# Kernel tuning notes

Measured on AMD Instinct MI355X. Metric: run time of the kernel, lower is better.

Reference implementation:

```python
import jax, jax.numpy as jnp
import numpy as np

B, NX, NY, E, H, L = 4, 1024, 1024, 512, 8, 4
DH = E // H
FF = 4 * E
SCALE = DH ** (-0.5)
EPS = 1e-5


def _ln(x, g, b):
    mu = jnp.mean(x, axis=-1, keepdims=True)
    var = jnp.mean((x - mu) ** 2, axis=-1, keepdims=True)
    return (x - mu) * jax.lax.rsqrt(var + EPS) * g + b


def setup_inputs() -> dict:
    key = jax.random.key(0)
    ks = jax.random.split(key, 16)
    s = 0.02
    inp = {
        'x': jax.random.normal(ks[0], (B, NX, E), jnp.float32),
        'y': jax.random.normal(ks[1], (B, NY, E), jnp.float32),
        'x_mask': jax.random.randint(ks[2], (B, NX), 0, 2, jnp.int32),
        'y_mask': jax.random.randint(ks[3], (B, NY), 0, 2, jnp.int32),
        # stacked per-layer params (L leading dim)
        'Wq': jax.random.normal(ks[4], (L, E, E), jnp.float32) * s,
        'bq': jnp.zeros((L, E), jnp.float32),
        'Wk': jax.random.normal(ks[5], (L, E, E), jnp.float32) * s,
        'bk': jnp.zeros((L, E), jnp.float32),
        'Wv': jax.random.normal(ks[6], (L, E, E), jnp.float32) * s,
        'bv': jnp.zeros((L, E), jnp.float32),
        'Wo': jax.random.normal(ks[7], (L, E, E), jnp.float32) * s,
        'bo': jnp.zeros((L, E), jnp.float32),
        'g1': jnp.ones((L, E), jnp.float32),
        'be1': jnp.zeros((L, E), jnp.float32),
        'g2': jnp.ones((L, E), jnp.float32),
        'be2': jnp.zeros((L, E), jnp.float32),
        'W1': jax.random.normal(ks[8], (L, E, FF), jnp.float32) * s,
        'bf1': jnp.zeros((L, FF), jnp.float32),
        'W2': jax.random.normal(ks[9], (L, FF, E), jnp.float32) * s,
        'bf2': jnp.zeros((L, E), jnp.float32),
    }
    return inp


def _forward(x, y, mask4, Wq, bq, Wk, bk, Wv, bv, Wo, bo, g1, be1, g2, be2, W1, bf1, W2, bf2):
    # mask4: (B,1,NX,NY) int, 0 = masked
    attn_prev = None
    out = x
    for l in range(L):
        q = x @ Wq[l] + bq[l]              # (B,NX,E)
        k = y @ Wk[l] + bk[l]
        v = y @ Wv[l] + bv[l]
        # faithful non-standard head split: plain reshape, no transpose
        q = q.reshape(B, H, NX, DH)
        k = k.reshape(B, H, NY, DH)
        v = v.reshape(B, H, NY, DH)
        scores = jnp.einsum('bhnd,bhmd->bhnm', q, k) * SCALE
        scores = jnp.where(mask4 == 0, jnp.float32(-1e9), scores)
        a = jax.nn.softmax(scores, axis=-1)
        if attn_prev is not None:
            a = a + attn_prev  # residual attention
        attn_prev = a
        o = jnp.einsum('bhnm,bhmd->bhnd', a, v)
        o = jnp.transpose(o, (0, 2, 1, 3)).reshape(B, NX, E)
        o = o @ Wo[l] + bo[l]
        h = _ln(x + o, g1[l], be1[l])
        ff = jax.nn.gelu(h @ W1[l] + bf1[l], approximate=False) @ W2[l] + bf2[l]
        out = _ln(h + ff, g2[l], be2[l])
        # NOTE: faithful to source, x and y are NOT updated between layers;
        # only the attention residual chains. Final output is last layer's out.
    return out


def reference(x, y, x_mask, y_mask, Wq, bq, Wk, bk, Wv, bv, Wo, bo, g1, be1, g2, be2, W1, bf1, W2, bf2):
    mask4 = (x_mask[:, :, None].astype(jnp.float32) @ y_mask[:, None, :].astype(jnp.float32)).astype(jnp.int32)[:, None]
    return _forward(x, y, mask4, Wq, bq, Wk, bk, Wv, bv, Wo, bo, g1, be1, g2, be2, W1, bf1, W2, bf2)
```

## Files before the change

kernel.cpp:

```cpp
#include <hip/hip_runtime.h>
#include <cstdint>

using u16    = unsigned short;
using u32    = unsigned int;
using bf16x8 = __attribute__((ext_vector_type(8))) __bf16;
using f32x4  = __attribute__((ext_vector_type(4))) float;

__device__ __forceinline__ u16 f2bf(float f) {
    u32 u = __builtin_bit_cast(u32, f);
    u += 0x7FFFu + ((u >> 16) & 1u);
    return (u16)(u >> 16);
}
__device__ __forceinline__ float bf2f(u16 u) {
    return __builtin_bit_cast(float, (u32)u << 16);
}
__device__ __forceinline__ u32 pk_bf16(float a, float b) {
    u32 r;
    asm("v_cvt_pk_bf16_f32 %0, %1, %2" : "=v"(r) : "v"(a), "v"(b));
    return r;
}
__device__ __forceinline__ float hw_exp2(float x) {
    float r;
    asm("v_exp_f32 %0, %1" : "=v"(r) : "v"(x));
    return r;
}
__device__ __forceinline__ void load_lds16(const u16* g, u16* l) {
    __builtin_amdgcn_global_load_lds((const __attribute__((address_space(1))) void*)g,
                                     (__attribute__((address_space(3))) void*)l, 16, 0, 0);
}

__global__ __launch_bounds__(256) void cvt2_kernel(const float* __restrict__ a,
                                                   const float* __restrict__ b,
                                                   u16* __restrict__ oa,
                                                   u16* __restrict__ ob)
{
    const int bid = blockIdx.x;
    const float* in = bid < 2048 ? a : b;
    u16* out = bid < 2048 ? oa : ob;
    int i = ((bid & 2047) * 256 + threadIdx.x) * 4;
    float4 v = *(const float4*)(in + i);
    uint2 o;
    o.x = (u32)f2bf(v.x) | ((u32)f2bf(v.y) << 16);
    o.y = (u32)f2bf(v.z) | ((u32)f2bf(v.w) << 16);
    *(uint2*)(out + i) = o;
}

__global__ __launch_bounds__(256) void wtrans_kernel(const float* __restrict__ Wq,
                                                     const float* __restrict__ Wk,
                                                     const float* __restrict__ Wv,
                                                     const float* __restrict__ Wo,
                                                     const float* __restrict__ W1,
                                                     const float* __restrict__ W2,
                                                     u16* __restrict__ wt)
{
    const int gid = blockIdx.x;
    const float* src; u16* dst; int K = 512, N = 512; int n0, k0;
    if (gid < 2560) {
        int z = gid >> 8, tid = gid & 255;
        switch (z) {
            case 0: case 1: case 2: case 3:
                src = Wq + (size_t)z * 262144;        dst = wt + (size_t)z * 262144;            break;
            case 4: case 5: case 6: case 7:
                src = Wk + (size_t)(z - 4) * 262144;  dst = wt + 1048576 + (size_t)(z - 4) * 262144; break;
            case 8: src = Wv + 3 * 262144;  dst = wt + 2097152; break;
            default: src = Wo + 3 * 262144; dst = wt + 2359296; break;
        }
        n0 = (tid & 15) * 32; k0 = (tid >> 4) * 32;
    } else if (gid < 3584) {
        int tid = gid - 2560;
        src = W1 + 3 * 1048576; dst = wt + 2621440; K = 512; N = 2048;
        n0 = (tid & 63) * 32; k0 = (tid >> 6) * 32;
    } else {
        int tid = gid - 3584;
        src = W2 + 3 * 1048576; dst = wt + 3670016; K = 2048; N = 512;
        n0 = (tid & 15) * 32; k0 = (tid >> 4) * 32;
    }
    __shared__ float tile[32][33];
    int tx = threadIdx.x, ty = threadIdx.y;
    #pragma unroll
    for (int i = 0; i < 4; i++) {
        int r = ty + i * 8;
        tile[r][tx] = src[(size_t)(k0 + r) * N + n0 + tx];
    }
    __syncthreads();
    #pragma unroll
    for (int i = 0; i < 4; i++) {
        int rn = ty + i * 8;
        dst[(size_t)(n0 + rn) * K + k0 + tx] = f2bf(tile[tx][rn]);
    }
}

template<int BNF>
__device__ __forceinline__ void gemm_core32(const u16* __restrict__ A,
                                            const u16* __restrict__ BT,
                                            int K, int m0, int n0,
                                            u16 (*As)[32], u16 (*Bs)[32],
                                            f32x4 acc[4][BNF])
{
    const int t    = threadIdx.x;
    const int lane = t & 63, wid = t >> 6;
    const int wm = wid >> 1, wn = wid & 1;
    const int lrow = lane & 15, kg = lane >> 4;
    const int sr = lane >> 2;
    const int sg = ((lane & 3) ^ ((lane >> 3) & 3)) * 8;

    auto stage = [&](int buf, int ks) {
        #pragma unroll
        for (int i = 0; i < 2; i++) {
            int row = wid * 32 + i * 16;
            load_lds16(&A[(size_t)(m0 + row + sr) * K + ks + sg], &As[buf * 128 + row][0]);
        }
        if constexpr (BNF == 4) {
            #pragma unroll
            for (int i = 0; i < 2; i++) {
                int row = wid * 32 + i * 16;
                load_lds16(&BT[(size_t)(n0 + row + sr) * K + ks + sg], &Bs[buf * 128 + row][0]);
            }
        } else {
            int row = wid * 16;
            load_lds16(&BT[(size_t)(n0 + row + sr) * K + ks + sg], &Bs[buf * 64 + row][0]);
        }
    };

    stage(0, 0);
    __syncthreads();
    int buf = 0;
    for (int ks = 0; ks < K; ks += 32) {
        if (ks + 32 < K) stage(buf ^ 1, ks + 32);
        const int rg = (kg ^ ((lrow >> 1) & 3)) * 8;
        bf16x8 af[4], bfv[BNF];
        #pragma unroll
        for (int i = 0; i < 4; i++)
            af[i] = *(const bf16x8*)&As[buf * 128 + wm * 64 + i * 16 + lrow][rg];
        #pragma unroll
        for (int j = 0; j < BNF; j++)
            bfv[j] = *(const bf16x8*)&Bs[buf * (BNF * 32) + wn * (BNF * 16) + j * 16 + lrow][rg];
        #pragma unroll
        for (int i = 0; i < 4; i++)
            #pragma unroll
            for (int j = 0; j < BNF; j++)
                acc[i][j] = __builtin_amdgcn_mfma_f32_16x16x32_bf16(af[i], bfv[j], acc[i][j], 0, 0, 0);
        __syncthreads();
        buf ^= 1;
    }
}

__global__ __launch_bounds__(256) void qkv_gemm_kernel(const u16* __restrict__ x16,
                                                       const u16* __restrict__ y16,
                                                       const u16* __restrict__ wt,
                                                       u16* __restrict__ qkv,
                                                       const float* __restrict__ bq,
                                                       const float* __restrict__ bk,
                                                       const float* __restrict__ bv,
                                                       const int* __restrict__ x_mask)
{
    __shared__ u16 As[256][32];
    __shared__ u16 Bs[256][32];
    const int z = blockIdx.z;
    const u16* A; const u16* BT; const float* bias;
    if (z < 4)      { A = x16; BT = wt + (size_t)z * 262144;                 bias = bq + z * 512; }
    else if (z < 8) { A = y16; BT = wt + 1048576 + (size_t)(z - 4) * 262144; bias = bk + (z - 4) * 512; }
    else            { A = y16; BT = wt + 2097152;                            bias = bv + 3 * 512; }
    u16* out = qkv + (size_t)z * 2097152;

    const int m0 = blockIdx.y * 128, n0 = blockIdx.x * 128;
    f32x4 acc[4][4];
    #pragma unroll
    for (int i = 0; i < 4; i++)
        #pragma unroll
        for (int j = 0; j < 4; j++) acc[i][j] = f32x4{0.f, 0.f, 0.f, 0.f};
    gemm_core32<4>(A, BT, 512, m0, n0, As, Bs, acc);

    const int lane = threadIdx.x & 63, wid = threadIdx.x >> 6;
    const int wm = wid >> 1, wn = wid & 1;
    const int lrow = lane & 15, kg = lane >> 4;
    #pragma unroll
    for (int i = 0; i < 4; i++)
        #pragma unroll
        for (int j = 0; j < 4; j++)
            #pragma unroll
            for (int r = 0; r < 4; r++) {
                int row = m0 + wm * 64 + i * 16 + kg * 4 + r;
                int col = n0 + wn * 64 + j * 16 + lrow;
                float v = acc[i][j][r] + bias[col];
                if (z < 4) v *= 0.180336880f * (x_mask[row] ? 1.f : 0.f);
                out[(size_t)row * 512 + col] = f2bf(v);
            }
}

template<int BNF, int EPI>
__global__ __launch_bounds__(256) void gemm_bt_kernel(const u16* __restrict__ A,
                                                      const u16* __restrict__ BT,
                                                      const float* __restrict__ bias,
                                                      void* __restrict__ outp,
                                                      const float* __restrict__ res,
                                                      int N, int K)
{
    __shared__ u16 As[256][32];
    __shared__ u16 Bs[BNF * 64][32];
    const int m0 = blockIdx.y * 128, n0 = blockIdx.x * (BNF * 32);
    f32x4 acc[4][BNF];
    #pragma unroll
    for (int i = 0; i < 4; i++)
        #pragma unroll
        for (int j = 0; j < BNF; j++) acc[i][j] = f32x4{0.f, 0.f, 0.f, 0.f};
    gemm_core32<BNF>(A, BT, K, m0, n0, As, Bs, acc);

    const int lane = threadIdx.x & 63, wid = threadIdx.x >> 6;
    const int wm = wid >> 1, wn = wid & 1;
    const int lrow = lane & 15, kg = lane >> 4;
    #pragma unroll
    for (int i = 0; i < 4; i++)
        #pragma unroll
        for (int j = 0; j < BNF; j++)
            #pragma unroll
            for (int r = 0; r < 4; r++) {
                int row = m0 + wm * 64 + i * 16 + kg * 4 + r;
                int col = n0 + wn * (BNF * 16) + j * 16 + lrow;
                float v = acc[i][j][r] + bias[col];
                if constexpr (EPI == 1) {
                    ((float*)outp)[(size_t)row * N + col] = v + res[(size_t)row * N + col];
                } else {
                    v = 0.5f * v * (1.f + erff(v * 0.70710678118654752f));
                    ((u16*)outp)[(size_t)row * N + col] = f2bf(v);
                }
            }
}

__global__ __launch_bounds__(256) void vtrans_kernel(const u16* __restrict__ v, u16* __restrict__ vt)
{
    const int bh = blockIdx.y, m0 = blockIdx.x * 64;
    const int b = bh >> 3, h = bh & 7;
    const u16* src = v + (size_t)b * 524288 + (size_t)h * 65536;
    u16* dst = vt + (size_t)bh * 65536;
    __shared__ u16 tile[64][72];
    const int t = threadIdx.x;
    #pragma unroll
    for (int i = 0; i < 2; i++) {
        int idx = t + i * 256, r = idx >> 3, q = idx & 7;
        *(uint4*)&tile[r][q * 8] = *(const uint4*)&src[(size_t)(m0 + r) * 64 + q * 8];
    }
    __syncthreads();
    #pragma unroll
    for (int i = 0; i < 2; i++) {
        int idx = t + i * 256, d = idx >> 3, q = idx & 7;
        alignas(16) u16 tmp[8];
        #pragma unroll
        for (int j = 0; j < 8; j++) tmp[j] = tile[q * 8 + j][d];
        *(uint4*)&dst[(size_t)d * 1024 + m0 + q * 8] = *(uint4*)tmp;
    }
}

__global__ __launch_bounds__(256, 2) void attn_kernel(const u16* __restrict__ qkv,
                                                      const int* __restrict__ x_mask,
                                                      const int* __restrict__ y_mask,
                                                      const u16* __restrict__ vt,
                                                      u16* __restrict__ obuf)
{
    __shared__ __align__(16) char smem[45056];
    u16 (*Kb)[4][32][64] = reinterpret_cast<u16(*)[4][32][64]>(smem);
    u16 (*Vb)[64][32]    = reinterpret_cast<u16(*)[64][32]>(smem + 32768);
    float* ymb           = reinterpret_cast<float*>(smem + 40960);
    u16 (*Osh)[64][72]   = reinterpret_cast<u16(*)[64][72]>(smem);

    const int t = threadIdx.x;
    const int wid = t >> 6, lane = t & 63;
    const int lrow = lane & 15, kg = lane >> 4;

    const int gid  = blockIdx.x;
    const int orig = (gid & 7) * 64 + (gid >> 3);
    const int bh = orig >> 4, qt = orig & 15;
    const int b = bh >> 3, h = bh & 7;
    const int q0 = qt * 64;

    const size_t headoff = (size_t)b * 524288 + (size_t)h * 65536;
    const u16* Q  = qkv + (size_t)wid * 2097152 + headoff;
    const u16* VT = vt + (size_t)bh * 65536;

    for (int i = t; i < 1024; i += 256)
        ymb[i] = y_mask[b * 1024 + i] ? 0.f : -1e9f;

    const int ksrow = wid * 8 + (lane >> 3);
    const int kscol = ((lane & 7) ^ (lane >> 3)) * 8;
    const int vsrow = wid * 16 + (lane >> 2);
    const int vscol = (((lane & 3) ^ ((vsrow & 3) ^ ((vsrow >> 2) & 3))) * 8);
    const int fswz  = (lrow & 3) ^ ((lrow >> 2) & 3);

    auto stage = [&](int buf, int mt) {
        const int m0 = mt * 32;
        #pragma unroll
        for (int it = 0; it < 4; it++) {
            const u16* src = qkv + (size_t)(4 + it) * 2097152 + headoff
                           + (size_t)(m0 + ksrow) * 64 + kscol;
            load_lds16(src, &Kb[buf][it][wid * 8][0]);
        }
        load_lds16(&VT[(size_t)vsrow * 1024 + m0 + vscol], &Vb[buf][wid * 16][0]);
    };

    bf16x8 aq[4][2];
    #pragma unroll
    for (int i = 0; i < 4; i++) {
        aq[i][0] = *(const bf16x8*)&Q[(size_t)(q0 + i * 16 + lrow) * 64 + kg * 8];
        aq[i][1] = *(const bf16x8*)&Q[(size_t)(q0 + i * 16 + lrow) * 64 + 32 + kg * 8];
    }
    float xmf[4];
    #pragma unroll
    for (int i = 0; i < 4; i++) xmf[i] = x_mask[b * 1024 + q0 + i * 16 + lrow] ? 1.f : 0.f;

    const int srcA = (((2 * kg) & 3) << 4) | lrow;
    const int srcB = (((2 * kg + 1) & 3) << 4) | lrow;

    f32x4 oacc[4][4];
    float psum[4] = {0.f, 0.f, 0.f, 0.f};
    #pragma unroll
    for (int i = 0; i < 4; i++)
        #pragma unroll
        for (int d = 0; d < 4; d++) oacc[i][d] = f32x4{0.f, 0.f, 0.f, 0.f};

    stage(0, 0);
    __syncthreads();

    for (int mt = 0; mt < 32; mt++) {
        const int buf = mt & 1;
        const int m0 = mt * 32;
        if (mt < 31) stage(buf ^ 1, mt + 1);

        bf16x8 kb[2][2];
        #pragma unroll
        for (int nf = 0; nf < 2; nf++)
            #pragma unroll
            for (int kk = 0; kk < 2; kk++)
                kb[nf][kk] = *(const bf16x8*)&Kb[buf][wid][nf * 16 + lrow][((kk * 4 + kg) ^ (lrow & 7)) * 8];

        float yb[2][4];
        #pragma unroll
        for (int nf = 0; nf < 2; nf++)
            #pragma unroll
            for (int r = 0; r < 4; r++) yb[nf][r] = ymb[m0 + nf * 16 + kg * 4 + r];

        bf16x8 pa[4];
        #pragma unroll
        for (int i = 0; i < 4; i++) {
            f32x4 s0 = f32x4{0.f, 0.f, 0.f, 0.f}, s1 = f32x4{0.f, 0.f, 0.f, 0.f};
            s0 = __builtin_amdgcn_mfma_f32_16x16x32_bf16(kb[0][0], aq[i][0], s0, 0, 0, 0);
            s0 = __builtin_amdgcn_mfma_f32_16x16x32_bf16(kb[0][1], aq[i][1], s0, 0, 0, 0);
            s1 = __builtin_amdgcn_mfma_f32_16x16x32_bf16(kb[1][0], aq[i][0], s1, 0, 0, 0);
            s1 = __builtin_amdgcn_mfma_f32_16x16x32_bf16(kb[1][1], aq[i][1], s1, 0, 0, 0);
            float p0 = hw_exp2(fmaf(xmf[i], yb[0][0], s0[0]));
            float p1 = hw_exp2(fmaf(xmf[i], yb[0][1], s0[1]));
            float p2 = hw_exp2(fmaf(xmf[i], yb[0][2], s0[2]));
            float p3 = hw_exp2(fmaf(xmf[i], yb[0][3], s0[3]));
            float p4 = hw_exp2(fmaf(xmf[i], yb[1][0], s1[0]));
            float p5 = hw_exp2(fmaf(xmf[i], yb[1][1], s1[1]));
            float p6 = hw_exp2(fmaf(xmf[i], yb[1][2], s1[2]));
            float p7 = hw_exp2(fmaf(xmf[i], yb[1][3], s1[3]));
            psum[i] += ((p0 + p1) + (p2 + p3)) + ((p4 + p5) + (p6 + p7));
            u32 w0 = pk_bf16(p0, p1), w1 = pk_bf16(p2, p3);
            u32 w2 = pk_bf16(p4, p5), w3 = pk_bf16(p6, p7);
            u32 a0 = __shfl(w0, srcA), a1 = __shfl(w1, srcA);
            u32 a2 = __shfl(w0, srcB), a3 = __shfl(w1, srcB);
            u32 b0 = __shfl(w2, srcA), b1 = __shfl(w3, srcA);
            u32 b2 = __shfl(w2, srcB), b3 = __shfl(w3, srcB);
            const bool hi = (kg & 2) != 0;
            uint4 pw;
            pw.x = hi ? b0 : a0;
            pw.y = hi ? b1 : a1;
            pw.z = hi ? b2 : a2;
            pw.w = hi ? b3 : a3;
            pa[i] = __builtin_bit_cast(bf16x8, pw);
        }

        bf16x8 vbf[4];
        #pragma unroll
        for (int d = 0; d < 4; d++)
            vbf[d] = *(const bf16x8*)&Vb[buf][d * 16 + lrow][(kg ^ fswz) * 8];
        #pragma unroll
        for (int i = 0; i < 4; i++)
            #pragma unroll
            for (int d = 0; d < 4; d++)
                oacc[i][d] = __builtin_amdgcn_mfma_f32_16x16x32_bf16(pa[i], vbf[d], oacc[i][d], 0, 0, 0);

        __syncthreads();
    }

    #pragma unroll
    for (int i = 0; i < 4; i++) {
        psum[i] += __shfl_xor(psum[i], 16);
        psum[i] += __shfl_xor(psum[i], 32);
    }
    float invr[4][4];
    #pragma unroll
    for (int i = 0; i < 4; i++) {
        float inv = 1.f / psum[i];
        #pragma unroll
        for (int r = 0; r < 4; r++) invr[i][r] = __shfl(inv, kg * 4 + r, 16);
    }

    #pragma unroll
    for (int i = 0; i < 4; i++)
        #pragma unroll
        for (int d = 0; d < 4; d++)
            #pragma unroll
            for (int r = 0; r < 4; r++)
                Osh[wid][i * 16 + kg * 4 + r][d * 16 + lrow] = f2bf(oacc[i][d][r] * invr[i][r]);
    __syncthreads();

    {
        const int row = t >> 2, cbase = (t & 3) * 16;
        #pragma unroll
        for (int half = 0; half < 2; half++) {
            const int c0 = cbase + half * 8;
            float a8[8] = {0, 0, 0, 0, 0, 0, 0, 0};
            #pragma unroll
            for (int l = 0; l < 4; l++) {
                uint4 v = *(const uint4*)&Osh[l][row][c0];
                const u16* pv = (const u16*)&v;
                #pragma unroll
                for (int j = 0; j < 8; j++) a8[j] += bf2f(pv[j]);
            }
            alignas(16) u16 tmp[8];
            #pragma unroll
            for (int j = 0; j < 8; j++) tmp[j] = f2bf(a8[j]);
            *(uint4*)&obuf[(size_t)(b * 1024 + q0 + row) * 512 + h * 64 + c0] = *(uint4*)tmp;
        }
    }
}

template<int MODE>
__global__ __launch_bounds__(256) void ln_kernel(const float* __restrict__ in,
                                                 const float* __restrict__ g,
                                                 const float* __restrict__ be,
                                                 float* __restrict__ out32,
                                                 u16* __restrict__ out16)
{
    const int wid = threadIdx.x >> 6, lane = threadIdx.x & 63;
    const int row = blockIdx.x * 4 + wid;
    const float* x = in + (size_t)row * 512;
    float4 v1 = *(const float4*)&x[lane * 8];
    float4 v2 = *(const float4*)&x[lane * 8 + 4];
    float xv[8] = { v1.x, v1.y, v1.z, v1.w, v2.x, v2.y, v2.z, v2.w };
    float s = 0.f, s2 = 0.f;
    #pragma unroll
    for (int j = 0; j < 8; j++) { s += xv[j]; s2 += xv[j] * xv[j]; }
    #pragma unroll
    for (int off = 32; off > 0; off >>= 1) {
        s  += __shfl_xor(s, off, 64);
        s2 += __shfl_xor(s2, off, 64);
    }
    const float mean = s * (1.f / 512.f);
    const float var  = s2 * (1.f / 512.f) - mean * mean;
    const float rstd = rsqrtf(var + 1e-5f);
    float ov[8];
    #pragma unroll
    for (int j = 0; j < 8; j++) {
        int col = lane * 8 + j;
        ov[j] = (xv[j] - mean) * rstd * g[col] + be[col];
    }
    *(float4*)&out32[(size_t)row * 512 + lane * 8]     = float4{ ov[0], ov[1], ov[2], ov[3] };
    *(float4*)&out32[(size_t)row * 512 + lane * 8 + 4] = float4{ ov[4], ov[5], ov[6], ov[7] };
    if constexpr (MODE == 0) {
        alignas(16) u16 tmp[8];
        #pragma unroll
        for (int j = 0; j < 8; j++) tmp[j] = f2bf(ov[j]);
        *(uint4*)&out16[(size_t)row * 512 + lane * 8] = *(uint4*)tmp;
    }
}

extern "C" void kernel_launch(void* const* d_in, const int* in_sizes, int n_in,
                              void* d_out, int out_size, void* d_ws, size_t ws_size,
                              hipStream_t stream) {
    const float* x      = (const float*)d_in[0];
    const float* y      = (const float*)d_in[1];
    const int*   x_mask = (const int*)d_in[2];
    const int*   y_mask = (const int*)d_in[3];
    const float* Wq  = (const float*)d_in[4];
    const float* bq  = (const float*)d_in[5];
    const float* Wk  = (const float*)d_in[6];
    const float* bk  = (const float*)d_in[7];
    const float* Wv  = (const float*)d_in[8];
    const float* bv  = (const float*)d_in[9];
    const float* Wo  = (const float*)d_in[10];
    const float* bo  = (const float*)d_in[11];
    const float* g1  = (const float*)d_in[12];
    const float* be1 = (const float*)d_in[13];
    const float* g2  = (const float*)d_in[14];
    const float* be2 = (const float*)d_in[15];
    const float* W1  = (const float*)d_in[16];
    const float* bf1 = (const float*)d_in[17];
    const float* W2  = (const float*)d_in[18];
    const float* bf2 = (const float*)d_in[19];

    char* p = (char*)d_ws;
    auto alloc = [&](size_t bytes) { char* r = p; p += (bytes + 255) & ~(size_t)255; return r; };
    u16*   x16   = (u16*)alloc(2097152ULL * 2);
    u16*   y16   = (u16*)alloc(2097152ULL * 2);
    u16*   wt    = (u16*)alloc(4718592ULL * 2);
    u16*   qkv   = (u16*)alloc(9ULL * 2097152 * 2);
    u16*   vt    = (u16*)alloc(2097152ULL * 2);
    u16*   obuf  = (u16*)alloc(2097152ULL * 2);
    float* xo    = (float*)alloc(2097152ULL * 4);
    float* h32   = (float*)alloc(2097152ULL * 4);
    u16*   h16   = (u16*)alloc(2097152ULL * 2);
    u16*   ffmid = (u16*)alloc(8388608ULL * 2);
    float* ffout = (float*)alloc(2097152ULL * 4);
    if ((size_t)(p - (char*)d_ws) > ws_size) return;

    cvt2_kernel<<<4096, 256, 0, stream>>>(x, y, x16, y16);
    wtrans_kernel<<<4608, dim3(32, 8), 0, stream>>>(Wq, Wk, Wv, Wo, W1, W2, wt);
    qkv_gemm_kernel<<<dim3(4, 32, 9), 256, 0, stream>>>(x16, y16, wt, qkv, bq, bk, bv, x_mask);
    vtrans_kernel<<<dim3(16, 32), 256, 0, stream>>>(qkv + 8ULL * 2097152, vt);
    attn_kernel<<<512, 256, 0, stream>>>(qkv, x_mask, y_mask, vt, obuf);
    gemm_bt_kernel<2, 1><<<dim3(8, 32), 256, 0, stream>>>(obuf, wt + 2359296, bo + 3 * 512, xo, x, 512, 512);
    ln_kernel<0><<<1024, 256, 0, stream>>>(xo, g1 + 3 * 512, be1 + 3 * 512, h32, h16);
    gemm_bt_kernel<4, 2><<<dim3(16, 32), 256, 0, stream>>>(h16, wt + 2621440, bf1 + 3 * 2048, ffmid, nullptr, 2048, 512);
    gemm_bt_kernel<2, 1><<<dim3(8, 32), 256, 0, stream>>>(ffmid, wt + 3670016, bf2 + 3 * 512, ffout, h32, 512, 2048);
    ln_kernel<1><<<1024, 256, 0, stream>>>(ffout, g2 + 3 * 512, be2 + 3 * 512, (float*)d_out, nullptr);
}
```

Before: 185.8 us.

## Split attention block into 8 waves covering two query halves

The attention kernel now launches 512 threads per block: each of four layer-waves is duplicated across two 32-row query halves, so each wave holds half the Q fragments and accumulators. K staging is spread over all 8 waves, and V staging uses only the first four. The final cross-layer sum is re-indexed so each thread reduces one 8-wide slice. This is meant to raise wave-level parallelism and cut per-wave register pressure. In exchange, K/V LDS reads are duplicated across the two query halves and the block barriers cover more waves.

```diff
diff --git a/kernel.cpp b/kernel.cpp
--- a/kernel.cpp
+++ b/kernel.cpp
@@ -251,21 +251,23 @@
     }
 }
 
-__global__ __launch_bounds__(256, 2) void attn_kernel(const u16* __restrict__ qkv,
-                                                      const int* __restrict__ x_mask,
-                                                      const int* __restrict__ y_mask,
-                                                      const u16* __restrict__ vt,
-                                                      u16* __restrict__ obuf)
+__global__ __launch_bounds__(512) void attn_kernel(const u16* __restrict__ qkv,
+                                                   const int* __restrict__ x_mask,
+                                                   const int* __restrict__ y_mask,
+                                                   const u16* __restrict__ vt,
+                                                   u16* __restrict__ obuf)
 {
     __shared__ __align__(16) char smem[45056];
     u16 (*Kb)[4][32][64] = reinterpret_cast<u16(*)[4][32][64]>(smem);
     u16 (*Vb)[64][32]    = reinterpret_cast<u16(*)[64][32]>(smem + 32768);
     float* ymb           = reinterpret_cast<float*>(smem + 40960);
-    u16 (*Osh)[64][72]   = reinterpret_cast<u16(*)[64][72]>(smem);
+    u16 (*Osh)[32][72]   = reinterpret_cast<u16(*)[32][72]>(smem);
 
     const int t = threadIdx.x;
     const int wid = t >> 6, lane = t & 63;
     const int lrow = lane & 15, kg = lane >> 4;
+    const int L  = wid & 3;
+    const int qh = wid >> 2;
 
     const int gid  = blockIdx.x;
     const int orig = (gid & 7) * 64 + (gid >> 3);
@@ -274,13 +276,12 @@
     const int q0 = qt * 64;
 
     const size_t headoff = (size_t)b * 524288 + (size_t)h * 65536;
-    const u16* Q  = qkv + (size_t)wid * 2097152 + headoff;
+    const u16* Q  = qkv + (size_t)L * 2097152 + headoff;
     const u16* VT = vt + (size_t)bh * 65536;
 
-    for (int i = t; i < 1024; i += 256)
+    for (int i = t; i < 1024; i += 512)
         ymb[i] = y_mask[b * 1024 + i] ? 0.f : -1e9f;
 
-    const int ksrow = wid * 8 + (lane >> 3);
     const int kscol = ((lane & 7) ^ (lane >> 3)) * 8;
     const int vsrow = wid * 16 + (lane >> 2);
     const int vscol = (((lane & 3) ^ ((vsrow & 3) ^ ((vsrow >> 2) & 3))) * 8);
@@ -288,32 +289,38 @@
 
     auto stage = [&](int buf, int mt) {
         const int m0 = mt * 32;
-        #pragma unroll
-        for (int it = 0; it < 4; it++) {
+        u16* kbase = &Kb[buf][0][0][0];
+        #pragma unroll
+        for (int i = 0; i < 2; i++) {
+            const int fr = i * 64 + wid * 8 + (lane >> 3);
+            const int it = fr >> 5, r = fr & 31;
             const u16* src = qkv + (size_t)(4 + it) * 2097152 + headoff
-                           + (size_t)(m0 + ksrow) * 64 + kscol;
-            load_lds16(src, &Kb[buf][it][wid * 8][0]);
+                           + (size_t)(m0 + r) * 64 + kscol;
+            load_lds16(src, kbase + (i * 512 + wid * 64) * 8);
         }
-        load_lds16(&VT[(size_t)vsrow * 1024 + m0 + vscol], &Vb[buf][wid * 16][0]);
+        if (wid < 4)
+            load_lds16(&VT[(size_t)vsrow * 1024 + m0 + vscol], &Vb[buf][wid * 16][0]);
     };
 
-    bf16x8 aq[4][2];
-    #pragma unroll
-    for (int i = 0; i < 4; i++) {
-        aq[i][0] = *(const bf16x8*)&Q[(size_t)(q0 + i * 16 + lrow) * 64 + kg * 8];
-        aq[i][1] = *(const bf16x8*)&Q[(size_t)(q0 + i * 16 + lrow) * 64 + 32 + kg * 8];
-    }
-    float xmf[4];
-    #pragma unroll
-    for (int i = 0; i < 4; i++) xmf[i] = x_mask[b * 1024 + q0 + i * 16 + lrow] ? 1.f : 0.f;
+    bf16x8 aq[2][2];
+    #pragma unroll
+    for (int i = 0; i < 2; i++) {
+        const int qr = q0 + qh * 32 + i * 16 + lrow;
+        aq[i][0] = *(const bf16x8*)&Q[(size_t)qr * 64 + kg * 8];
+        aq[i][1] = *(const bf16x8*)&Q[(size_t)qr * 64 + 32 + kg * 8];
+    }
+    float xmf[2];
+    #pragma unroll
+    for (int i = 0; i < 2; i++)
+        xmf[i] = x_mask[b * 1024 + q0 + qh * 32 + i * 16 + lrow] ? 1.f : 0.f;
 
     const int srcA = (((2 * kg) & 3) << 4) | lrow;
     const int srcB = (((2 * kg + 1) & 3) << 4) | lrow;
 
-    f32x4 oacc[4][4];
-    float psum[4] = {0.f, 0.f, 0.f, 0.f};
-    #pragma unroll
-    for (int i = 0; i < 4; i++)
+    f32x4 oacc[2][4];
+    float psum[2] = {0.f, 0.f};
+    #pragma unroll
+    for (int i = 0; i < 2; i++)
         #pragma unroll
         for (int d = 0; d < 4; d++) oacc[i][d] = f32x4{0.f, 0.f, 0.f, 0.f};
 
@@ -330,7 +337,7 @@
         for (int nf = 0; nf < 2; nf++)
             #pragma unroll
             for (int kk = 0; kk < 2; kk++)
-                kb[nf][kk] = *(const bf16x8*)&Kb[buf][wid][nf * 16 + lrow][((kk * 4 + kg) ^ (lrow & 7)) * 8];
+                kb[nf][kk] = *(const bf16x8*)&Kb[buf][L][nf * 16 + lrow][((kk * 4 + kg) ^ (lrow & 7)) * 8];
 
         float yb[2][4];
         #pragma unroll
@@ -338,9 +345,9 @@
             #pragma unroll
             for (int r = 0; r < 4; r++) yb[nf][r] = ymb[m0 + nf * 16 + kg * 4 + r];
 
-        bf16x8 pa[4];
-        #pragma unroll
-        for (int i = 0; i < 4; i++) {
+        bf16x8 pa[2];
+        #pragma unroll
+        for (int i = 0; i < 2; i++) {
             f32x4 s0 = f32x4{0.f, 0.f, 0.f, 0.f}, s1 = f32x4{0.f, 0.f, 0.f, 0.f};
             s0 = __builtin_amdgcn_mfma_f32_16x16x32_bf16(kb[0][0], aq[i][0], s0, 0, 0, 0);
             s0 = __builtin_amdgcn_mfma_f32_16x16x32_bf16(kb[0][1], aq[i][1], s0, 0, 0, 0);
@@ -375,7 +382,7 @@
         for (int d = 0; d < 4; d++)
             vbf[d] = *(const bf16x8*)&Vb[buf][d * 16 + lrow][(kg ^ fswz) * 8];
         #pragma unroll
-        for (int i = 0; i < 4; i++)
+        for (int i = 0; i < 2; i++)
             #pragma unroll
             for (int d = 0; d < 4; d++)
                 oacc[i][d] = __builtin_amdgcn_mfma_f32_16x16x32_bf16(pa[i], vbf[d], oacc[i][d], 0, 0, 0);
@@ -384,20 +391,20 @@
     }
 
     #pragma unroll
-    for (int i = 0; i < 4; i++) {
+    for (int i = 0; i < 2; i++) {
         psum[i] += __shfl_xor(psum[i], 16);
         psum[i] += __shfl_xor(psum[i], 32);
     }
-    float invr[4][4];
-    #pragma unroll
-    for (int i = 0; i < 4; i++) {
+    float invr[2][4];
+    #pragma unroll
+    for (int i = 0; i < 2; i++) {
         float inv = 1.f / psum[i];
         #pragma unroll
         for (int r = 0; r < 4; r++) invr[i][r] = __shfl(inv, kg * 4 + r, 16);
     }
 
     #pragma unroll
-    for (int i = 0; i < 4; i++)
+    for (int i = 0; i < 2; i++)
         #pragma unroll
         for (int d = 0; d < 4; d++)
             #pragma unroll
@@ -406,23 +413,20 @@
     __syncthreads();
 
     {
-        const int row = t >> 2, cbase = (t & 3) * 16;
-        #pragma unroll
-        for (int half = 0; half < 2; half++) {
-            const int c0 = cbase + half * 8;
-            float a8[8] = {0, 0, 0, 0, 0, 0, 0, 0};
-            #pragma unroll
-            for (int l = 0; l < 4; l++) {
-                uint4 v = *(const uint4*)&Osh[l][row][c0];
-                const u16* pv = (const u16*)&v;
-                #pragma unroll
-                for (int j = 0; j < 8; j++) a8[j] += bf2f(pv[j]);
-            }
-            alignas(16) u16 tmp[8];
-            #pragma unroll
-            for (int j = 0; j < 8; j++) tmp[j] = f2bf(a8[j]);
-            *(uint4*)&obuf[(size_t)(b * 1024 + q0 + row) * 512 + h * 64 + c0] = *(uint4*)tmp;
+        const int row64 = t >> 3, c0 = (t & 7) * 8;
+        const int wbase = (row64 >> 5) * 4, lr = row64 & 31;
+        float a8[8] = {0, 0, 0, 0, 0, 0, 0, 0};
+        #pragma unroll
+        for (int l = 0; l < 4; l++) {
+            uint4 v = *(const uint4*)&Osh[wbase + l][lr][c0];
+            const u16* pv = (const u16*)&v;
+            #pragma unroll
+            for (int j = 0; j < 8; j++) a8[j] += bf2f(pv[j]);
         }
+        alignas(16) u16 tmp[8];
+        #pragma unroll
+        for (int j = 0; j < 8; j++) tmp[j] = f2bf(a8[j]);
+        *(uint4*)&obuf[(size_t)(b * 1024 + q0 + row64) * 512 + h * 64 + c0] = *(uint4*)tmp;
     }
 }
 
@@ -509,7 +513,7 @@
     wtrans_kernel<<<4608, dim3(32, 8), 0, stream>>>(Wq, Wk, Wv, Wo, W1, W2, wt);
     qkv_gemm_kernel<<<dim3(4, 32, 9), 256, 0, stream>>>(x16, y16, wt, qkv, bq, bk, bv, x_mask);
     vtrans_kernel<<<dim3(16, 32), 256, 0, stream>>>(qkv + 8ULL * 2097152, vt);
-    attn_kernel<<<512, 256, 0, stream>>>(qkv, x_mask, y_mask, vt, obuf);
+    attn_kernel<<<512, 512, 0, stream>>>(qkv, x_mask, y_mask, vt, obuf);
     gemm_bt_kernel<2, 1><<<dim3(8, 32), 256, 0, stream>>>(obuf, wt + 2359296, bo + 3 * 512, xo, x, 512, 512);
     ln_kernel<0><<<1024, 256, 0, stream>>>(xo, g1 + 3 * 512, be1 + 3 * 512, h32, h16);
     gemm_bt_kernel<4, 2><<<dim3(16, 32), 256, 0, stream>>>(h16, wt + 2621440, bf1 + 3 * 2048, ffmid, nullptr, 2048, 512);
```

After: 185.3 us. Within noise of the previous version (-0.3%).
